# Optimization experiments

Hardware: AMD Instinct MI355X
Metric: run time of the kernel (lower is better)

The kernel has to match this reference:

```python
import jax, jax.numpy as jnp
import numpy as np

K = 3  # polynomial filter order

def gfgcn_layer(X, S, W, h, b):
    # X: [N, in], W: [in, out], h: [K], b: [out]
    X = X @ W
    X_out = h[0] * X
    Sx = X
    for k in range(1, K):
        Sx = S @ Sx                 # graph shift propagation
        X_out = X_out + h[k] * Sx   # scalar-weighted accumulate
    return X_out + b[None, :]


def setup_inputs() -> dict:
    key = jax.random.key(0)
    ks = jax.random.split(key, 12)
    N, in_dim, hid_dim, out_dim = 8192, 512, 128, 64
    # scale S so repeated propagation stays numerically tame
    S = jax.random.normal(ks[0], (N, N), dtype=jnp.float32) / jnp.sqrt(jnp.float32(N))
    X = jax.random.normal(ks[1], (N, in_dim), dtype=jnp.float32)
    def kaiming(k, shape):
        bound = np.sqrt(6.0 / shape[0])
        return jax.random.uniform(k, shape, jnp.float32, -bound, bound)
    W1 = kaiming(ks[2], (in_dim, hid_dim))
    W2 = kaiming(ks[3], (hid_dim, hid_dim))
    W3 = kaiming(ks[4], (hid_dim, out_dim))
    h1 = jnp.ones((K,), jnp.float32)
    h2 = jnp.ones((K,), jnp.float32)
    h3 = jnp.ones((K,), jnp.float32)
    b1 = jnp.zeros((hid_dim,), jnp.float32)
    b2 = jnp.zeros((hid_dim,), jnp.float32)
    b3 = jnp.zeros((out_dim,), jnp.float32)
    return {"S": S, "X": X, "W1": W1, "h1": h1, "b1": b1,
            "W2": W2, "h2": h2, "b2": b2, "W3": W3, "h3": h3, "b3": b3}


def reference(S, X, W1, h1, b1, W2, h2, b2, W3, h3, b3):
    # layer 1 + ReLU (dropout p=0 -> identity, batch_norm=False)
    X = jax.nn.relu(gfgcn_layer(X, S, W1, h1, b1))
    # layer 2 + ReLU
    X = jax.nn.relu(gfgcn_layer(X, S, W2, h2, b2))
    # last layer, last_act = Identity
    return gfgcn_layer(X, S, W3, h3, b3)
```

## Files before the change

kernel.cpp:

```cpp
#include <hip/hip_runtime.h>


typedef __attribute__((ext_vector_type(4))) float  f32x4;
typedef __attribute__((ext_vector_type(8))) __bf16 bf16x8;
typedef __attribute__((ext_vector_type(4))) __bf16 bf16x4;

__device__ __forceinline__ void gload_lds16(const __bf16* g, __bf16* l) {
    __builtin_amdgcn_global_load_lds(
        (const __attribute__((address_space(1))) void*)g,
        (__attribute__((address_space(3))) void*)l, 16, 0, 0);
}

__global__ __launch_bounds__(256)
void pack_S(const float* __restrict__ S, __bf16* __restrict__ Spk,
            int KCH, int SP) {
    __shared__ __bf16 L[8][1032];
    const int t = threadIdx.x;
    const int m = blockIdx.x, z = blockIdx.y;
    __bf16* tile = Spk + ((size_t)m * SP + z) * ((size_t)64 * KCH);

    const int rl    = t & 7;
    const int cstep = t >> 3;
    const int stl0  = t >> 5;
    const int slot  = t & 31;
    const int rs    = slot >> 2;
    const int q     = slot & 3;

    for (int r0 = 0; r0 < 64; r0 += 8) {
        const int rg_st = r0 + rs;
        const int qq    = q ^ ((rg_st >> 1) & 3);
        for (int c1 = 0; c1 < KCH; c1 += 1024) {
            const float* src = S + (size_t)(m * 64 + r0 + rl) * 8192
                                 + (size_t)z * KCH + c1 + cstep * 32;
            #pragma unroll
            for (int j = 0; j < 4; j++) {
                float4 f0 = *(const float4*)(src + j * 8);
                float4 f1 = *(const float4*)(src + j * 8 + 4);
                bf16x8 v;
                v[0]=(__bf16)f0.x; v[1]=(__bf16)f0.y; v[2]=(__bf16)f0.z; v[3]=(__bf16)f0.w;
                v[4]=(__bf16)f1.x; v[5]=(__bf16)f1.y; v[6]=(__bf16)f1.z; v[7]=(__bf16)f1.w;
                *(bf16x8*)&L[rl][cstep * 32 + j * 8] = v;
            }
            __syncthreads();
            #pragma unroll
            for (int k2 = 0; k2 < 4; k2++) {
                const int stl = stl0 + k2 * 8;
                bf16x8 v = *(const bf16x8*)&L[rs][stl * 32 + qq * 8];
                *(bf16x8*)(tile + (size_t)((c1 >> 5) + stl) * 2048
                                + (size_t)(r0 * 4 + slot) * 8) = v;
            }
            __syncthreads();
        }
    }
}

__global__ void cvt_transpose(const float* __restrict__ W,
                              __bf16* __restrict__ Wt, int Kd, int Md) {
    int i = blockIdx.x * blockDim.x + threadIdx.x;
    if (i < Kd * Md) {
        int k = i / Md, m = i % Md;
        Wt[(size_t)m * Kd + k] = (__bf16)W[i];
    }
}

template<int MF, int NF, int OUTMODE, int BF32>
__global__ __launch_bounds__(256)
void gemm_rd(const __bf16* __restrict__ A, const void* __restrict__ Bv,
             void* __restrict__ out, int K, int Kchunk, int Mtot, int Ntot)
{
    const int lane = threadIdx.x & 63;
    const int w    = threadIdx.x >> 6;
    const int l15  = lane & 15;
    const int quad = lane >> 4;

    const int m_base = blockIdx.x * (64 * MF) + w * (16 * MF);
    const int n_base = blockIdx.y * (16 * NF);
    const int kstart = blockIdx.z * Kchunk;

    const __bf16* Ap[MF];
    #pragma unroll
    for (int mf = 0; mf < MF; mf++)
        Ap[mf] = A + (size_t)(m_base + mf * 16 + l15) * K + kstart + quad * 8;

    const __bf16* Bp[NF];
    const float*  Bpf[NF];
    #pragma unroll
    for (int nf = 0; nf < NF; nf++) {
        const size_t roff = (size_t)(n_base + nf * 16 + l15) * K + kstart + quad * 8;
        if (BF32) Bpf[nf] = (const float*)Bv + roff;
        else      Bp[nf]  = (const __bf16*)Bv + roff;
    }

    f32x4 acc[MF][NF];
    #pragma unroll
    for (int mf = 0; mf < MF; mf++)
        #pragma unroll
        for (int nf = 0; nf < NF; nf++)
            acc[mf][nf] = (f32x4){0.f, 0.f, 0.f, 0.f};

    #pragma unroll 2
    for (int ks = 0; ks < Kchunk; ks += 32) {
        bf16x8 a[MF], b[NF];
        #pragma unroll
        for (int mf = 0; mf < MF; mf++) a[mf] = *(const bf16x8*)(Ap[mf] + ks);
        #pragma unroll
        for (int nf = 0; nf < NF; nf++) {
            if (BF32) {
                float4 f0 = *(const float4*)(Bpf[nf] + ks);
                float4 f1 = *(const float4*)(Bpf[nf] + ks + 4);
                bf16x8 tt;
                tt[0] = (__bf16)f0.x; tt[1] = (__bf16)f0.y;
                tt[2] = (__bf16)f0.z; tt[3] = (__bf16)f0.w;
                tt[4] = (__bf16)f1.x; tt[5] = (__bf16)f1.y;
                tt[6] = (__bf16)f1.z; tt[7] = (__bf16)f1.w;
                b[nf] = tt;
            } else {
                b[nf] = *(const bf16x8*)(Bp[nf] + ks);
            }
        }
        #pragma unroll
        for (int mf = 0; mf < MF; mf++)
            #pragma unroll
            for (int nf = 0; nf < NF; nf++)
                acc[mf][nf] = __builtin_amdgcn_mfma_f32_16x16x32_bf16(
                    a[mf], b[nf], acc[mf][nf], 0, 0, 0);
    }

    if (OUTMODE == 0) {
        float* P = (float*)out + (size_t)blockIdx.z * Mtot * Ntot;
        #pragma unroll
        for (int mf = 0; mf < MF; mf++) {
            const int rowb = m_base + mf * 16 + quad * 4;
            #pragma unroll
            for (int nf = 0; nf < NF; nf++) {
                const int col = n_base + nf * 16 + l15;
                *(f32x4*)(P + (size_t)col * Mtot + rowb) = acc[mf][nf];
            }
        }
    } else {
        __bf16* O = (__bf16*)out;
        #pragma unroll
        for (int mf = 0; mf < MF; mf++) {
            const int rowb = m_base + mf * 16 + quad * 4;
            #pragma unroll
            for (int nf = 0; nf < NF; nf++) {
                const int col = n_base + nf * 16 + l15;
                #pragma unroll
                for (int r = 0; r < 4; r++)
                    O[(size_t)(rowb + r) * Ntot + col] = (__bf16)acc[mf][nf][r];
            }
        }
    }
}

template<int NFW>
__global__ __launch_bounds__(256)
void sgemm_lds(const __bf16* __restrict__ Spk, const __bf16* __restrict__ Bt,
               float* __restrict__ P, int Kb, int Kchunk, int Mtot)
{
    constexpr int BN = 32 * NFW;
    __shared__ __bf16 Asm[3][64 * 32];
    __shared__ __bf16 Bsm[3][BN * 32];

    const int t    = threadIdx.x;
    const int lane = t & 63;
    const int w    = t >> 6;
    const int wm   = w >> 1;
    const int wn   = w & 1;
    const int l15  = lane & 15;
    const int quad = lane >> 4;

    const int m_block = blockIdx.x * 64;
    const int kstart  = blockIdx.z * Kchunk;
    const int nst     = Kchunk >> 5;

    const __bf16* gApk = Spk
        + ((size_t)blockIdx.x * gridDim.z + blockIdx.z) * ((size_t)64 * Kchunk);

    const int rt  = t >> 2;
    const int qs  = (t & 3) ^ ((rt >> 1) & 3);
    const __bf16* gB0 = Bt + (size_t)rt * Kb        + kstart + qs * 8;
    const __bf16* gB1 = Bt + (size_t)(64 + rt) * Kb + kstart + qs * 8;

    f32x4 acc[2][NFW];
    #pragma unroll
    for (int mf = 0; mf < 2; mf++)
        #pragma unroll
        for (int nf = 0; nf < NFW; nf++)
            acc[mf][nf] = (f32x4){0.f, 0.f, 0.f, 0.f};

    auto stage = [&](int buf, int st) {
        gload_lds16(gApk + (size_t)st * 2048 + t * 8, &Asm[buf][t * 8]);
        const int ks = st << 5;
        gload_lds16(gB0 + ks, &Bsm[buf][t * 8]);
        if (NFW == 4)
            gload_lds16(gB1 + ks, &Bsm[buf][2048 + t * 8]);
    };

    int aoff[2], boff[NFW];
    #pragma unroll
    for (int mf = 0; mf < 2; mf++) {
        const int ar = wm * 32 + mf * 16 + l15;
        aoff[mf] = ar * 32 + (quad ^ ((ar >> 1) & 3)) * 8;
    }
    #pragma unroll
    for (int nf = 0; nf < NFW; nf++) {
        const int br = wn * 16 * NFW + nf * 16 + l15;
        boff[nf] = br * 32 + (quad ^ ((br >> 1) & 3)) * 8;
    }

    stage(0, 0);
    if (nst > 1) stage(1, 1);
    if (nst > 2) stage(2, 2);

    for (int st = 0; st < nst; ++st) {
        const int rem   = nst - 1 - st;
        const int ahead = rem < 2 ? rem : 2;

        if (ahead == 2) {
            if (NFW == 4) asm volatile("s_waitcnt vmcnt(6)" ::: "memory");
            else          asm volatile("s_waitcnt vmcnt(4)" ::: "memory");
        } else if (ahead == 1) {
            if (NFW == 4) asm volatile("s_waitcnt vmcnt(3)" ::: "memory");
            else          asm volatile("s_waitcnt vmcnt(2)" ::: "memory");
        } else {
            asm volatile("s_waitcnt vmcnt(0)" ::: "memory");
        }
        __builtin_amdgcn_s_barrier();
        asm volatile("" ::: "memory");

        const int buf = st - (st / 3) * 3;
        bf16x8 a[2], b[NFW];
        #pragma unroll
        for (int mf = 0; mf < 2; mf++)
            a[mf] = *(const bf16x8*)&Asm[buf][aoff[mf]];
        #pragma unroll
        for (int nf = 0; nf < NFW; nf++)
            b[nf] = *(const bf16x8*)&Bsm[buf][boff[nf]];

        asm volatile("s_waitcnt lgkmcnt(0)" ::: "memory");
        __builtin_amdgcn_s_barrier();
        asm volatile("" ::: "memory");
        if (st + 3 < nst) stage(buf, st + 3);

        #pragma unroll
        for (int mf = 0; mf < 2; mf++)
            #pragma unroll
            for (int nf = 0; nf < NFW; nf++)
                acc[mf][nf] = __builtin_amdgcn_mfma_f32_16x16x32_bf16(
                    a[mf], b[nf], acc[mf][nf], 0, 0, 0);
    }

    float* Pz = P + (size_t)blockIdx.z * Mtot * BN;
    #pragma unroll
    for (int mf = 0; mf < 2; mf++) {
        const int rowb = m_block + wm * 32 + mf * 16 + quad * 4;
        #pragma unroll
        for (int nf = 0; nf < NFW; nf++) {
            const int col = wn * 16 * NFW + nf * 16 + l15;
            *(f32x4*)(Pz + (size_t)col * Mtot + rowb) = acc[mf][nf];
        }
    }
}

__global__ void reduce_partials(const float* __restrict__ P,
                                __bf16* __restrict__ Y, int total4,
                                int SP, int MN) {
    int i = blockIdx.x * blockDim.x + threadIdx.x;
    if (i >= total4) return;
    size_t base = (size_t)i * 4;
    float4 s = *(const float4*)(P + base);
    for (int sp = 1; sp < SP; sp++) {
        float4 v = *(const float4*)(P + (size_t)sp * MN + base);
        s.x += v.x; s.y += v.y; s.z += v.z; s.w += v.w;
    }
    bf16x4 o; o[0] = (__bf16)s.x; o[1] = (__bf16)s.y;
    o[2] = (__bf16)s.z; o[3] = (__bf16)s.w;
    *(bf16x4*)(Y + base) = o;
}

template<int RELU, int F32OUT>
__global__ void combine_out(const float* __restrict__ P,
                            const __bf16* __restrict__ Y0t,
                            const __bf16* __restrict__ Y1t,
                            const float* __restrict__ h,
                            const float* __restrict__ bias,
                            void* __restrict__ outp,
                            int F, int SP) {
    const int i = blockIdx.x * blockDim.x + threadIdx.x;
    const int total = F * 2048;
    if (i >= total) return;
    const int f  = i >> 11;
    const int n4 = i & 2047;
    const size_t base = (size_t)f * 8192 + (size_t)n4 * 4;
    const int MN = F * 8192;

    float4 s = *(const float4*)(P + base);
    for (int sp = 1; sp < SP; sp++) {
        float4 v = *(const float4*)(P + (size_t)sp * MN + base);
        s.x += v.x; s.y += v.y; s.z += v.z; s.w += v.w;
    }
    bf16x4 y0 = *(const bf16x4*)(Y0t + base);
    bf16x4 y1 = *(const bf16x4*)(Y1t + base);
    const float h0 = h[0], h1 = h[1], h2 = h[2], bb = bias[f];

    float v[4] = {s.x, s.y, s.z, s.w};
    #pragma unroll
    for (int r = 0; r < 4; r++) {
        float x = h0 * (float)y0[r] + h1 * (float)y1[r] + h2 * v[r] + bb;
        if (RELU) x = fmaxf(x, 0.0f);
        v[r] = x;
    }
    const int node = n4 * 4;
    if (F32OUT) {
        float* O = (float*)outp;
        #pragma unroll
        for (int r = 0; r < 4; r++) O[(size_t)(node + r) * F + f] = v[r];
    } else {
        __bf16* O = (__bf16*)outp;
        #pragma unroll
        for (int r = 0; r < 4; r++) O[(size_t)(node + r) * F + f] = (__bf16)v[r];
    }
}

extern "C" void kernel_launch(void* const* d_in, const int* in_sizes, int n_in,
                              void* d_out, int out_size, void* d_ws, size_t ws_size,
                              hipStream_t stream) {
    const float* S  = (const float*)d_in[0];
    const float* X  = (const float*)d_in[1];
    const float* W1 = (const float*)d_in[2];
    const float* h1 = (const float*)d_in[3];
    const float* b1 = (const float*)d_in[4];
    const float* W2 = (const float*)d_in[5];
    const float* h2 = (const float*)d_in[6];
    const float* b2 = (const float*)d_in[7];
    const float* W3 = (const float*)d_in[8];
    const float* h3 = (const float*)d_in[9];
    const float* b3 = (const float*)d_in[10];
    float* out = (float*)d_out;

    const int Nn = 8192, IN = 512, HID = 128, OUT = 64;

    char* ws = (char*)d_ws;
    size_t off = 0;
    auto carve = [&](size_t bytes) -> void* {
        void* p = ws + off;
        off += (bytes + 255) & ~(size_t)255;
        return p;
    };
    __bf16* Spk = (__bf16*)carve((size_t)Nn * Nn  * 2);
    __bf16* W1t = (__bf16*)carve((size_t)IN  * HID * 2);
    __bf16* W2t = (__bf16*)carve((size_t)HID * HID * 2);
    __bf16* W3t = (__bf16*)carve((size_t)HID * OUT * 2);
    __bf16* Y0t = (__bf16*)carve((size_t)HID * Nn * 2);
    __bf16* Y1t = (__bf16*)carve((size_t)HID * Nn * 2);
    __bf16* Act = (__bf16*)carve((size_t)Nn * HID * 2);
    size_t  base = off;

    const size_t per_split = (size_t)HID * Nn * 4;
    int SP = 1;
    while (SP < 8 && base + (size_t)(SP * 2) * per_split <= ws_size) SP *= 2;
    float* P = (float*)carve((size_t)SP * per_split);
    const int KCH = Nn / SP;

    pack_S<<<dim3(Nn / 64, SP), dim3(256), 0, stream>>>(S, Spk, KCH, SP);
    cvt_transpose<<<dim3((IN * HID + 255) / 256), dim3(256), 0, stream>>>(W1, W1t, IN, HID);
    cvt_transpose<<<dim3((HID * HID + 255) / 256), dim3(256), 0, stream>>>(W2, W2t, HID, HID);
    cvt_transpose<<<dim3((HID * OUT + 255) / 256), dim3(256), 0, stream>>>(W3, W3t, HID, OUT);

    auto sgemm = [&](const __bf16* Bt, int F) {
        if (F == 128)
            sgemm_lds<4><<<dim3(Nn / 64, 1, SP), dim3(256), 0, stream>>>(
                Spk, Bt, P, Nn, KCH, Nn);
        else
            sgemm_lds<2><<<dim3(Nn / 64, 1, SP), dim3(256), 0, stream>>>(
                Spk, Bt, P, Nn, KCH, Nn);
    };
    auto reduceY = [&](__bf16* Y, int F) {
        int t4 = F * 2048;
        reduce_partials<<<dim3((t4 + 255) / 256), dim3(256), 0, stream>>>(
            P, Y, t4, SP, F * Nn);
    };

    gemm_rd<2, 4, 1, 1><<<dim3(1, Nn / 64, 1), dim3(256), 0, stream>>>(
        W1t, X, Y0t, IN, IN, HID, Nn);
    sgemm(Y0t, HID);
    reduceY(Y1t, HID);
    sgemm(Y1t, HID);
    combine_out<1, 0><<<dim3(HID * 2048 / 256), dim3(256), 0, stream>>>(
        P, Y0t, Y1t, h1, b1, Act, HID, SP);

    gemm_rd<2, 4, 1, 0><<<dim3(1, Nn / 64, 1), dim3(256), 0, stream>>>(
        W2t, Act, Y0t, HID, HID, HID, Nn);
    sgemm(Y0t, HID);
    reduceY(Y1t, HID);
    sgemm(Y1t, HID);
    combine_out<1, 0><<<dim3(HID * 2048 / 256), dim3(256), 0, stream>>>(
        P, Y0t, Y1t, h2, b2, Act, HID, SP);

    gemm_rd<1, 4, 1, 0><<<dim3(1, Nn / 64, 1), dim3(256), 0, stream>>>(
        W3t, Act, Y0t, HID, HID, OUT, Nn);
    sgemm(Y0t, OUT);
    reduceY(Y1t, OUT);
    sgemm(Y1t, OUT);
    combine_out<0, 1><<<dim3(OUT * 2048 / 256), dim3(256), 0, stream>>>(
        P, Y0t, Y1t, h3, b3, out, OUT, SP);

    (void)in_sizes; (void)n_in; (void)out_size;
}
```

Baseline: 695.5 us.

## Replace 4-wave S-GEMM with single-wave blocks and deeper 5-stage prefetch

The S propagation GEMM now uses one 64-thread wave per block, computing the whole 64xBN tile. This removes all block barriers and deepens the LDS async prefetch ring from 3 to 5 stages. The K-split factor is capped at 4 instead of 8, which halves partial-sum traffic and reduction work but leaves fewer blocks in the grid. Each wave now holds 4xNFW accumulators (up to 32 f32x4), which raises register pressure, and occupancy depends on LDS per block.

Result: slower. 734.0 us (+5.5%).

```diff
diff --git a/kernel.cpp b/kernel.cpp
--- a/kernel.cpp
+++ b/kernel.cpp
@@ -154,21 +154,18 @@
 }
 
 template<int NFW>
-__global__ __launch_bounds__(256)
-void sgemm_lds(const __bf16* __restrict__ Spk, const __bf16* __restrict__ Bt,
-               float* __restrict__ P, int Kb, int Kchunk, int Mtot)
+__global__ __launch_bounds__(64)
+void sgemm_1w(const __bf16* __restrict__ Spk, const __bf16* __restrict__ Bt,
+              float* __restrict__ P, int Kb, int Kchunk, int Mtot)
 {
-    constexpr int BN = 32 * NFW;
-    __shared__ __bf16 Asm[3][64 * 32];
-    __shared__ __bf16 Bsm[3][BN * 32];
+    constexpr int DEPTH = 5;
+    constexpr int BN = NFW * 16;
+    __shared__ __bf16 Asm[DEPTH][64 * 32];
+    __shared__ __bf16 Bsm[DEPTH][BN * 32];
 
     const int t    = threadIdx.x;
-    const int lane = t & 63;
-    const int w    = t >> 6;
-    const int wm   = w >> 1;
-    const int wn   = w & 1;
-    const int l15  = lane & 15;
-    const int quad = lane >> 4;
+    const int l15  = t & 15;
+    const int quad = t >> 4;
 
     const int m_block = blockIdx.x * 64;
     const int kstart  = blockIdx.z * Kchunk;
@@ -177,87 +174,94 @@
     const __bf16* gApk = Spk
         + ((size_t)blockIdx.x * gridDim.z + blockIdx.z) * ((size_t)64 * Kchunk);
 
-    const int rt  = t >> 2;
-    const int qs  = (t & 3) ^ ((rt >> 1) & 3);
-    const __bf16* gB0 = Bt + (size_t)rt * Kb        + kstart + qs * 8;
-    const __bf16* gB1 = Bt + (size_t)(64 + rt) * Kb + kstart + qs * 8;
-
-    f32x4 acc[2][NFW];
-    #pragma unroll
-    for (int mf = 0; mf < 2; mf++)
+    const __bf16* gB[NFW];
+    #pragma unroll
+    for (int r = 0; r < NFW; r++) {
+        const int br = r * 16 + (t >> 2);
+        const int qs = (t & 3) ^ ((br >> 1) & 3);
+        gB[r] = Bt + (size_t)br * Kb + kstart + qs * 8;
+    }
+
+    f32x4 acc[4][NFW];
+    #pragma unroll
+    for (int mf = 0; mf < 4; mf++)
         #pragma unroll
         for (int nf = 0; nf < NFW; nf++)
             acc[mf][nf] = (f32x4){0.f, 0.f, 0.f, 0.f};
 
+    int aoff[4], boff[NFW];
+    #pragma unroll
+    for (int mf = 0; mf < 4; mf++) {
+        const int ar = mf * 16 + l15;
+        aoff[mf] = ar * 32 + (quad ^ ((ar >> 1) & 3)) * 8;
+    }
+    #pragma unroll
+    for (int nf = 0; nf < NFW; nf++) {
+        const int br = nf * 16 + l15;
+        boff[nf] = br * 32 + (quad ^ ((br >> 1) & 3)) * 8;
+    }
+
     auto stage = [&](int buf, int st) {
-        gload_lds16(gApk + (size_t)st * 2048 + t * 8, &Asm[buf][t * 8]);
-        const int ks = st << 5;
-        gload_lds16(gB0 + ks, &Bsm[buf][t * 8]);
-        if (NFW == 4)
-            gload_lds16(gB1 + ks, &Bsm[buf][2048 + t * 8]);
+        #pragma unroll
+        for (int r = 0; r < 4; r++)
+            gload_lds16(gApk + (size_t)st * 2048 + r * 512 + t * 8,
+                        &Asm[buf][r * 512 + t * 8]);
+        #pragma unroll
+        for (int r = 0; r < NFW; r++)
+            gload_lds16(gB[r] + (size_t)st * 32,
+                        &Bsm[buf][r * 512 + t * 8]);
     };
 
-    int aoff[2], boff[NFW];
-    #pragma unroll
-    for (int mf = 0; mf < 2; mf++) {
-        const int ar = wm * 32 + mf * 16 + l15;
-        aoff[mf] = ar * 32 + (quad ^ ((ar >> 1) & 3)) * 8;
-    }
-    #pragma unroll
-    for (int nf = 0; nf < NFW; nf++) {
-        const int br = wn * 16 * NFW + nf * 16 + l15;
-        boff[nf] = br * 32 + (quad ^ ((br >> 1) & 3)) * 8;
-    }
-
-    stage(0, 0);
-    if (nst > 1) stage(1, 1);
-    if (nst > 2) stage(2, 2);
-
+    #pragma unroll
+    for (int s = 0; s < DEPTH; s++)
+        if (s < nst) stage(s, s);
+
+    int buf = 0;
     for (int st = 0; st < nst; ++st) {
         const int rem   = nst - 1 - st;
-        const int ahead = rem < 2 ? rem : 2;
-
-        if (ahead == 2) {
-            if (NFW == 4) asm volatile("s_waitcnt vmcnt(6)" ::: "memory");
-            else          asm volatile("s_waitcnt vmcnt(4)" ::: "memory");
-        } else if (ahead == 1) {
-            if (NFW == 4) asm volatile("s_waitcnt vmcnt(3)" ::: "memory");
-            else          asm volatile("s_waitcnt vmcnt(2)" ::: "memory");
+        const int ahead = rem < (DEPTH - 1) ? rem : (DEPTH - 1);
+        if (NFW == 8) {
+            if      (ahead >= 4) asm volatile("s_waitcnt vmcnt(48)" ::: "memory");
+            else if (ahead == 3) asm volatile("s_waitcnt vmcnt(36)" ::: "memory");
+            else if (ahead == 2) asm volatile("s_waitcnt vmcnt(24)" ::: "memory");
+            else if (ahead == 1) asm volatile("s_waitcnt vmcnt(12)" ::: "memory");
+            else                 asm volatile("s_waitcnt vmcnt(0)"  ::: "memory");
         } else {
-            asm volatile("s_waitcnt vmcnt(0)" ::: "memory");
-        }
-        __builtin_amdgcn_s_barrier();
-        asm volatile("" ::: "memory");
-
-        const int buf = st - (st / 3) * 3;
-        bf16x8 a[2], b[NFW];
-        #pragma unroll
-        for (int mf = 0; mf < 2; mf++)
+            if      (ahead >= 4) asm volatile("s_waitcnt vmcnt(32)" ::: "memory");
+            else if (ahead == 3) asm volatile("s_waitcnt vmcnt(24)" ::: "memory");
+            else if (ahead == 2) asm volatile("s_waitcnt vmcnt(16)" ::: "memory");
+            else if (ahead == 1) asm volatile("s_waitcnt vmcnt(8)"  ::: "memory");
+            else                 asm volatile("s_waitcnt vmcnt(0)"  ::: "memory");
+        }
+
+        bf16x8 a[4], b[NFW];
+        #pragma unroll
+        for (int mf = 0; mf < 4; mf++)
             a[mf] = *(const bf16x8*)&Asm[buf][aoff[mf]];
         #pragma unroll
         for (int nf = 0; nf < NFW; nf++)
             b[nf] = *(const bf16x8*)&Bsm[buf][boff[nf]];
 
         asm volatile("s_waitcnt lgkmcnt(0)" ::: "memory");
-        __builtin_amdgcn_s_barrier();
-        asm volatile("" ::: "memory");
-        if (st + 3 < nst) stage(buf, st + 3);
-
-        #pragma unroll
-        for (int mf = 0; mf < 2; mf++)
+        if (st + DEPTH < nst) stage(buf, st + DEPTH);
+
+        #pragma unroll
+        for (int mf = 0; mf < 4; mf++)
             #pragma unroll
             for (int nf = 0; nf < NFW; nf++)
                 acc[mf][nf] = __builtin_amdgcn_mfma_f32_16x16x32_bf16(
                     a[mf], b[nf], acc[mf][nf], 0, 0, 0);
+
+        buf = (buf + 1 == DEPTH) ? 0 : buf + 1;
     }
 
     float* Pz = P + (size_t)blockIdx.z * Mtot * BN;
     #pragma unroll
-    for (int mf = 0; mf < 2; mf++) {
-        const int rowb = m_block + wm * 32 + mf * 16 + quad * 4;
+    for (int mf = 0; mf < 4; mf++) {
+        const int rowb = m_block + mf * 16 + quad * 4;
         #pragma unroll
         for (int nf = 0; nf < NFW; nf++) {
-            const int col = wn * 16 * NFW + nf * 16 + l15;
+            const int col = nf * 16 + l15;
             *(f32x4*)(Pz + (size_t)col * Mtot + rowb) = acc[mf][nf];
         }
     }
@@ -359,7 +363,7 @@
 
     const size_t per_split = (size_t)HID * Nn * 4;
     int SP = 1;
-    while (SP < 8 && base + (size_t)(SP * 2) * per_split <= ws_size) SP *= 2;
+    while (SP < 4 && base + (size_t)(SP * 2) * per_split <= ws_size) SP *= 2;
     float* P = (float*)carve((size_t)SP * per_split);
     const int KCH = Nn / SP;
 
@@ -370,10 +374,10 @@
 
     auto sgemm = [&](const __bf16* Bt, int F) {
         if (F == 128)
-            sgemm_lds<4><<<dim3(Nn / 64, 1, SP), dim3(256), 0, stream>>>(
+            sgemm_1w<8><<<dim3(Nn / 64, 1, SP), dim3(64), 0, stream>>>(
                 Spk, Bt, P, Nn, KCH, Nn);
         else
-            sgemm_lds<2><<<dim3(Nn / 64, 1, SP), dim3(256), 0, stream>>>(
+            sgemm_1w<4><<<dim3(Nn / 64, 1, SP), dim3(64), 0, stream>>>(
                 Spk, Bt, P, Nn, KCH, Nn);
     };
     auto reduceY = [&](__bf16* Y, int F) {
```

## Add 512-thread S-propagation GEMM for 128-wide features with 8 waves

Applied to the files above, without the earlier changes.

Adds a new sgemm_lds8 kernel that computes the 64x128 output tile with 8 waves (2x4 layout, 2x2 MFMA fragments per wave) instead of 4 waves, and routes the F=128 propagation calls to it. It keeps the triple-buffered LDS pipeline, with per-wave vmcnt waits adjusted because only half the threads load A. The gemm_rd epilogue is also simplified to always write bf16 output. The aim is more waves per tile to hide latency in the memory-bound S@X pass, at the cost of fewer accumulators per wave and more barrier contention.

Measured after the change: 696.5 us. About the same (+0.1%).

```diff
diff --git a/kernel.cpp b/kernel.cpp
--- a/kernel.cpp
+++ b/kernel.cpp
@@ -126,29 +126,122 @@
                     a[mf], b[nf], acc[mf][nf], 0, 0, 0);
     }
 
-    if (OUTMODE == 0) {
-        float* P = (float*)out + (size_t)blockIdx.z * Mtot * Ntot;
-        #pragma unroll
-        for (int mf = 0; mf < MF; mf++) {
-            const int rowb = m_base + mf * 16 + quad * 4;
+    __bf16* O = (__bf16*)out;
+    #pragma unroll
+    for (int mf = 0; mf < MF; mf++) {
+        const int rowb = m_base + mf * 16 + quad * 4;
+        #pragma unroll
+        for (int nf = 0; nf < NF; nf++) {
+            const int col = n_base + nf * 16 + l15;
             #pragma unroll
-            for (int nf = 0; nf < NF; nf++) {
-                const int col = n_base + nf * 16 + l15;
-                *(f32x4*)(P + (size_t)col * Mtot + rowb) = acc[mf][nf];
-            }
-        }
-    } else {
-        __bf16* O = (__bf16*)out;
-        #pragma unroll
-        for (int mf = 0; mf < MF; mf++) {
-            const int rowb = m_base + mf * 16 + quad * 4;
+            for (int r = 0; r < 4; r++)
+                O[(size_t)(rowb + r) * Ntot + col] = (__bf16)acc[mf][nf][r];
+        }
+    }
+    (void)Mtot; (void)OUTMODE;
+}
+
+__global__ __launch_bounds__(512)
+void sgemm_lds8(const __bf16* __restrict__ Spk, const __bf16* __restrict__ Bt,
+                float* __restrict__ P, int Kb, int Kchunk, int Mtot)
+{
+    __shared__ __bf16 Asm[3][64 * 32];
+    __shared__ __bf16 Bsm[3][128 * 32];
+
+    const int t    = threadIdx.x;
+    const int lane = t & 63;
+    const int w    = t >> 6;
+    const int wm   = w >> 2;
+    const int wn   = w & 3;
+    const int l15  = lane & 15;
+    const int quad = lane >> 4;
+
+    const int m_block = blockIdx.x * 64;
+    const int kstart  = blockIdx.z * Kchunk;
+    const int nst     = Kchunk >> 5;
+
+    const __bf16* gApk = Spk
+        + ((size_t)blockIdx.x * gridDim.z + blockIdx.z) * ((size_t)64 * Kchunk);
+
+    const int rt  = t >> 2;
+    const int qs  = (t & 3) ^ ((rt >> 1) & 3);
+    const __bf16* gB = Bt + (size_t)rt * Kb + kstart + qs * 8;
+
+    f32x4 acc[2][2];
+    #pragma unroll
+    for (int mf = 0; mf < 2; mf++)
+        #pragma unroll
+        for (int nf = 0; nf < 2; nf++)
+            acc[mf][nf] = (f32x4){0.f, 0.f, 0.f, 0.f};
+
+    auto stage = [&](int buf, int st) {
+        if (t < 256)
+            gload_lds16(gApk + (size_t)st * 2048 + t * 8, &Asm[buf][t * 8]);
+        gload_lds16(gB + (st << 5), &Bsm[buf][t * 8]);
+    };
+
+    int aoff[2], boff[2];
+    #pragma unroll
+    for (int mf = 0; mf < 2; mf++) {
+        const int ar = wm * 32 + mf * 16 + l15;
+        aoff[mf] = ar * 32 + (quad ^ ((ar >> 1) & 3)) * 8;
+    }
+    #pragma unroll
+    for (int nf = 0; nf < 2; nf++) {
+        const int br = wn * 32 + nf * 16 + l15;
+        boff[nf] = br * 32 + (quad ^ ((br >> 1) & 3)) * 8;
+    }
+
+    stage(0, 0);
+    if (nst > 1) stage(1, 1);
+    if (nst > 2) stage(2, 2);
+
+    for (int st = 0; st < nst; ++st) {
+        const int rem   = nst - 1 - st;
+        const int ahead = rem < 2 ? rem : 2;
+
+        if (w < 4) {
+            if      (ahead == 2) asm volatile("s_waitcnt vmcnt(4)" ::: "memory");
+            else if (ahead == 1) asm volatile("s_waitcnt vmcnt(2)" ::: "memory");
+            else                 asm volatile("s_waitcnt vmcnt(0)" ::: "memory");
+        } else {
+            if      (ahead == 2) asm volatile("s_waitcnt vmcnt(2)" ::: "memory");
+            else if (ahead == 1) asm volatile("s_waitcnt vmcnt(1)" ::: "memory");
+            else                 asm volatile("s_waitcnt vmcnt(0)" ::: "memory");
+        }
+        __builtin_amdgcn_s_barrier();
+        asm volatile("" ::: "memory");
+
+        const int buf = st - (st / 3) * 3;
+        bf16x8 a[2], b[2];
+        #pragma unroll
+        for (int mf = 0; mf < 2; mf++)
+            a[mf] = *(const bf16x8*)&Asm[buf][aoff[mf]];
+        #pragma unroll
+        for (int nf = 0; nf < 2; nf++)
+            b[nf] = *(const bf16x8*)&Bsm[buf][boff[nf]];
+
+        asm volatile("s_waitcnt lgkmcnt(0)" ::: "memory");
+        __builtin_amdgcn_s_barrier();
+        asm volatile("" ::: "memory");
+        if (st + 3 < nst) stage(buf, st + 3);
+
+        #pragma unroll
+        for (int mf = 0; mf < 2; mf++)
             #pragma unroll
-            for (int nf = 0; nf < NF; nf++) {
-                const int col = n_base + nf * 16 + l15;
-                #pragma unroll
-                for (int r = 0; r < 4; r++)
-                    O[(size_t)(rowb + r) * Ntot + col] = (__bf16)acc[mf][nf][r];
-            }
+            for (int nf = 0; nf < 2; nf++)
+                acc[mf][nf] = __builtin_amdgcn_mfma_f32_16x16x32_bf16(
+                    a[mf], b[nf], acc[mf][nf], 0, 0, 0);
+    }
+
+    float* Pz = P + (size_t)blockIdx.z * Mtot * 128;
+    #pragma unroll
+    for (int mf = 0; mf < 2; mf++) {
+        const int rowb = m_block + wm * 32 + mf * 16 + quad * 4;
+        #pragma unroll
+        for (int nf = 0; nf < 2; nf++) {
+            const int col = wn * 32 + nf * 16 + l15;
+            *(f32x4*)(Pz + (size_t)col * Mtot + rowb) = acc[mf][nf];
         }
     }
 }
@@ -370,7 +463,7 @@
 
     auto sgemm = [&](const __bf16* Bt, int F) {
         if (F == 128)
-            sgemm_lds<4><<<dim3(Nn / 64, 1, SP), dim3(256), 0, stream>>>(
+            sgemm_lds8<<<dim3(Nn / 64, 1, SP), dim3(512), 0, stream>>>(
                 Spk, Bt, P, Nn, KCH, Nn);
         else
             sgemm_lds<2><<<dim3(Nn / 64, 1, SP), dim3(256), 0, stream>>>(
```
